# Kernel tuning notes

Hardware: AMD Instinct MI355X
Metric: run time of the kernel (lower is better)

Reference implementation:

```python
import jax, jax.numpy as jnp
import numpy as np

B, HH, WW, C, HEADS = 8, 56, 56, 384, 6
DIM_OUT = 384


def _upsample2x_bilinear(x):
    # x: [..., m, n] -> [..., 2m, 2n]; matches torch F.interpolate bilinear align_corners=False
    m, n = x.shape[-2], x.shape[-1]
    def coords(inn):
        c = (jnp.arange(2 * inn) + 0.5) / 2.0 - 0.5
        c = jnp.clip(c, 0.0, inn - 1)
        i0 = jnp.floor(c).astype(jnp.int32)
        i1 = jnp.minimum(i0 + 1, inn - 1)
        return i0, i1, (c - i0).astype(x.dtype)
    i0, i1, wy = coords(m)
    j0, j1, wx = coords(n)
    rows = x[..., i0, :] * (1 - wy)[:, None] + x[..., i1, :] * wy[:, None]
    return rows[..., :, j0] * (1 - wx) + rows[..., :, j1] * wx


def setup_inputs() -> dict:
    key = jax.random.key(0)
    ks = jax.random.split(key, 12)
    inp = {
        'x': jax.random.normal(ks[0], (B, HH * WW, C), jnp.float32),
        'res_attn': jax.random.normal(ks[1], (B, HEADS, (HH // 4) * (WW // 4), (HH // 2) * (WW // 2)), jnp.float32),
        'conv_q_w': jax.random.normal(ks[2], (C, 1, 3, 3), jnp.float32) * 0.05,
        'ln_g': jnp.ones((C,), jnp.float32),
        'ln_b': jnp.zeros((C,), jnp.float32),
        'wq': jax.random.normal(ks[3], (DIM_OUT, C), jnp.float32) * 0.02,
        'wk': jax.random.normal(ks[4], (DIM_OUT, C), jnp.float32) * 0.02,
        'wv': jax.random.normal(ks[5], (DIM_OUT, C), jnp.float32) * 0.02,
        'w_proj': jax.random.normal(ks[6], (DIM_OUT, DIM_OUT), jnp.float32) * 0.02,
        'b_proj': jnp.zeros((DIM_OUT,), jnp.float32),
        'w_fuse': jax.random.normal(ks[7], (HEADS, 2 * HEADS, 1, 1), jnp.float32) * 0.1,
        'b_fuse': jnp.zeros((HEADS,), jnp.float32),
        'h': HH,
        'w': WW,
    }
    return inp


def reference(x, res_attn, conv_q_w, ln_g, ln_b, wq, wk, wv, w_proj, b_proj, w_fuse, b_fuse, h, w):
    Bz, _, Cc = x.shape
    heads = w_fuse.shape[0]
    xi = x.transpose(0, 2, 1).reshape(Bz, Cc, h, w)  # b c h w
    # conv_proj_q: depthwise conv k3 s2 p1 (no bias), then LayerNorm
    q = jax.lax.conv_general_dilated(
        xi, conv_q_w, (2, 2), ((1, 1), (1, 1)),
        dimension_numbers=('NCHW', 'OIHW', 'NCHW'), feature_group_count=Cc)
    hq, wq2 = q.shape[2], q.shape[3]
    q = q.reshape(Bz, Cc, hq * wq2).transpose(0, 2, 1)  # b t c
    mu = q.mean(-1, keepdims=True)
    var = ((q - mu) ** 2).mean(-1, keepdims=True)
    q = (q - mu) / jnp.sqrt(var + 1e-5) * ln_g + ln_b
    # conv_proj_k/v: avg pool k2 s2 p0
    kv = xi.reshape(Bz, Cc, h // 2, 2, w // 2, 2).mean(axis=(3, 5))
    kv = kv.reshape(Bz, Cc, (h // 2) * (w // 2)).transpose(0, 2, 1)  # b t c
    dim_out = wq.shape[0]
    dh = dim_out // heads
    def split(t):
        return t.reshape(Bz, t.shape[1], heads, dh).transpose(0, 2, 1, 3)
    qh = split(q @ wq.T)
    kh = split(kv @ wk.T)
    vh = split(kv @ wv.T)
    scale = dim_out ** -0.5
    attn_score = jnp.einsum('bhlk,bhtk->bhlt', qh, kh) * scale  # [B,H,L,T]
    sh, sw = h // 4, w // 4
    a = res_attn.shape[-1]
    rx = res_attn[:, :, :sh * sw, :]
    rx = rx.reshape(Bz * heads, sh * sw, a).transpose(0, 2, 1).reshape(Bz * heads, a, sh, sw)
    rx = _upsample2x_bilinear(rx)  # (b h) a 2sh 2sw
    rx = rx.reshape(Bz, heads, a, 4 * sh * sw).transpose(0, 1, 3, 2)  # b h L a
    cat = jnp.concatenate([attn_score, rx], axis=1)  # [B, 2H, L, T]
    attn_score = jnp.einsum('bclt,oc->bolt', cat, w_fuse[:, :, 0, 0]) + b_fuse[None, :, None, None]
    attn = jax.nn.softmax(attn_score, axis=-1)
    out = jnp.einsum('bhlt,bhtv->bhlv', attn, vh)
    out = out.transpose(0, 2, 1, 3).reshape(Bz, -1, dim_out)
    return out @ w_proj.T + b_proj
```

## Files before the change

kernel.cpp:

```cpp
#include <hip/hip_runtime.h>

typedef unsigned int uint;
typedef unsigned short ushort_t;
typedef short bf16x8 __attribute__((ext_vector_type(8)));
typedef float f32x4 __attribute__((ext_vector_type(4)));

__device__ __forceinline__ ushort_t f2bf(float f) {
  uint u = __builtin_bit_cast(uint, f);
  u += 0x7fffu + ((u >> 16) & 1u);
  return (ushort_t)(u >> 16);
}
__device__ __forceinline__ float bf2f(ushort_t s) {
  return __builtin_bit_cast(float, (uint)s << 16);
}
__device__ __forceinline__ bf16x8 ld_frag(const ushort_t* p) {
  return __builtin_bit_cast(bf16x8, *(const uint4*)p);
}

__global__ __launch_bounds__(384) void k_convln(
    const float* __restrict__ x, const float* __restrict__ wc,
    const float* __restrict__ g, const float* __restrict__ bb,
    ushort_t* __restrict__ qout)
{
  const int b  = blockIdx.x / 784;
  const int t  = blockIdx.x % 784;
  const int oy = t / 28, ox = t % 28;
  const int c  = threadIdx.x;
  const float* xb = x + (size_t)b * 3136 * 384 + c;
  float acc = 0.f;
  #pragma unroll
  for (int ky = 0; ky < 3; ky++) {
    const int iy = 2 * oy - 1 + ky;
    if (iy < 0 || iy >= 56) continue;
    #pragma unroll
    for (int kx = 0; kx < 3; kx++) {
      const int ix = 2 * ox - 1 + kx;
      if (ix < 0 || ix >= 56) continue;
      acc += wc[c * 9 + ky * 3 + kx] * xb[(size_t)(iy * 56 + ix) * 384];
    }
  }
  float s = acc, s2 = acc * acc;
  #pragma unroll
  for (int off = 32; off >= 1; off >>= 1) {
    s  += __shfl_xor(s,  off);
    s2 += __shfl_xor(s2, off);
  }
  __shared__ float ps[6], ps2[6];
  if ((c & 63) == 0) { ps[c >> 6] = s; ps2[c >> 6] = s2; }
  __syncthreads();
  float S = 0.f, S2 = 0.f;
  #pragma unroll
  for (int i = 0; i < 6; i++) { S += ps[i]; S2 += ps2[i]; }
  const float mu  = S * (1.f / 384.f);
  const float var = S2 * (1.f / 384.f) - mu * mu;
  const float inv = rsqrtf(var + 1e-5f);
  qout[((size_t)b * 784 + t) * 384 + c] = f2bf((acc - mu) * inv * g[c] + bb[c]);
}

__global__ __launch_bounds__(256) void k_pool(
    const float* __restrict__ x, ushort_t* __restrict__ kvout)
{
  const int idx = blockIdx.x * 256 + threadIdx.x;
  const int c = idx % 384;
  const int t = (idx / 384) % 784;
  const int b = idx / (384 * 784);
  const int ty = t / 28, tx = t % 28;
  const float* xb = x + (size_t)b * 3136 * 384 + c;
  const int r0 = (2 * ty) * 56 + 2 * tx;
  const float v = xb[(size_t)r0 * 384] + xb[(size_t)(r0 + 1) * 384]
                + xb[(size_t)(r0 + 56) * 384] + xb[(size_t)(r0 + 57) * 384];
  kvout[idx] = f2bf(v * 0.25f);
}

__global__ __launch_bounds__(256) void k_wcvt(
    const float* __restrict__ a, const float* __restrict__ b,
    const float* __restrict__ c, const float* __restrict__ d,
    ushort_t* __restrict__ oa, ushort_t* __restrict__ ob,
    ushort_t* __restrict__ oc, ushort_t* __restrict__ od)
{
  const int i = blockIdx.x * 256 + threadIdx.x;
  if (i < 147456) {
    oa[i] = f2bf(a[i]); ob[i] = f2bf(b[i]);
    oc[i] = f2bf(c[i]); od[i] = f2bf(d[i]);
  }
}

template<int MODE>
__global__ __launch_bounds__(256) void k_gemm(
    const ushort_t* __restrict__ X, const ushort_t* __restrict__ W,
    const float* __restrict__ bias, void* __restrict__ Y)
{
  __shared__ ushort_t As[128][40];
  __shared__ ushort_t Bs[128][40];
  const int tid = threadIdx.x, w = tid >> 6, lane = tid & 63;
  const int quad = lane >> 4, r = lane & 15;
  const int m0 = blockIdx.y * 128, n0 = blockIdx.x * 128;
  const int wm = w >> 1, wn = w & 1;
  const int lr = tid >> 2, lc = (tid & 3) << 3;
  const ushort_t* xp = X + (size_t)(m0 + lr) * 384 + lc;
  const ushort_t* wp = W + (size_t)(n0 + lr) * 384 + lc;
  f32x4 acc[4][4] = {};
  for (int k0 = 0; k0 < 384; k0 += 32) {
    __syncthreads();
    *(uint4*)&As[lr][lc]      = *(const uint4*)(xp + k0);
    *(uint4*)&As[lr + 64][lc] = *(const uint4*)(xp + (size_t)64 * 384 + k0);
    *(uint4*)&Bs[lr][lc]      = *(const uint4*)(wp + k0);
    *(uint4*)&Bs[lr + 64][lc] = *(const uint4*)(wp + (size_t)64 * 384 + k0);
    __syncthreads();
    bf16x8 af[4], bf_[4];
    #pragma unroll
    for (int mt = 0; mt < 4; mt++) af[mt]  = *(const bf16x8*)&As[wm * 64 + mt * 16 + r][quad * 8];
    #pragma unroll
    for (int nt = 0; nt < 4; nt++) bf_[nt] = *(const bf16x8*)&Bs[wn * 64 + nt * 16 + r][quad * 8];
    #pragma unroll
    for (int mt = 0; mt < 4; mt++)
      #pragma unroll
      for (int nt = 0; nt < 4; nt++)
        acc[mt][nt] = __builtin_amdgcn_mfma_f32_16x16x32_bf16(af[mt], bf_[nt], acc[mt][nt], 0, 0, 0);
  }
  #pragma unroll
  for (int mt = 0; mt < 4; mt++) {
    #pragma unroll
    for (int nt = 0; nt < 4; nt++) {
      #pragma unroll
      for (int i = 0; i < 4; i++) {
        const int row = m0 + wm * 64 + mt * 16 + quad * 4 + i;
        const int col = n0 + wn * 64 + nt * 16 + r;
        const float v = acc[mt][nt][i];
        if constexpr (MODE == 2) {
          ((float*)Y)[(size_t)row * 384 + col] = v + bias[col];
        } else if constexpr (MODE == 0) {
          ((ushort_t*)Y)[(size_t)row * 384 + col] = f2bf(v);
        } else {
          const int bb = row / 784, tt = row % 784;
          ((ushort_t*)Y)[((size_t)bb * 384 + col) * 784 + tt] = f2bf(v);
        }
      }
    }
  }
}

__global__ __launch_bounds__(256) void k_qk(
    const ushort_t* __restrict__ Qb, const ushort_t* __restrict__ Kb,
    ushort_t* __restrict__ S)
{
  const int tid = threadIdx.x, w = tid >> 6, lane = tid & 63;
  const int quad = lane >> 4, r = lane & 15;
  const int bh = blockIdx.z, b = bh / 6, h = bh % 6;
  const int m0 = blockIdx.y * 64 + w * 16;
  const int t0 = blockIdx.x * 112;
  const int lq = min(m0 + r, 783);
  const ushort_t* qp = Qb + (size_t)(b * 784 + lq) * 384 + h * 64 + quad * 8;
  const bf16x8 a0 = ld_frag(qp), a1 = ld_frag(qp + 32);
  f32x4 acc[7] = {};
  #pragma unroll
  for (int j = 0; j < 7; j++) {
    const int t = t0 + j * 16 + r;
    const ushort_t* kp = Kb + (size_t)(b * 784 + t) * 384 + h * 64 + quad * 8;
    acc[j] = __builtin_amdgcn_mfma_f32_16x16x32_bf16(a0, ld_frag(kp),      acc[j], 0, 0, 0);
    acc[j] = __builtin_amdgcn_mfma_f32_16x16x32_bf16(a1, ld_frag(kp + 32), acc[j], 0, 0, 0);
  }
  const float scale = 0.05103103630798288f;
  #pragma unroll
  for (int j = 0; j < 7; j++) {
    #pragma unroll
    for (int i = 0; i < 4; i++) {
      const int lo = m0 + quad * 4 + i;
      if (lo < 784)
        S[((size_t)(b * 784 + lo) * 6 + h) * 784 + t0 + j * 16 + r] = f2bf(acc[j][i] * scale);
    }
  }
}

__global__ __launch_bounds__(256) void k_fuse(
    ushort_t* __restrict__ S, const float* __restrict__ ra,
    const float* __restrict__ w_fuse, const float* __restrict__ b_fuse)
{
  const int tid = threadIdx.x;
  const int bl = blockIdx.x, b = bl / 784, l = bl % 784;
  __shared__ float wf[72], bfu[6];
  __shared__ float redm[4][6], reds[4][6];
  if (tid < 72) wf[tid] = w_fuse[tid];
  if (tid < 6)  bfu[tid] = b_fuse[tid];
  __syncthreads();

  const int Y = l / 28, X = l % 28;
  const float cy = fminf(fmaxf((float)Y * 0.5f - 0.25f, 0.f), 13.f);
  const float cx = fminf(fmaxf((float)X * 0.5f - 0.25f, 0.f), 13.f);
  const int y0 = (int)cy, y1 = min(y0 + 1, 13);
  const int x0 = (int)cx, x1 = min(x0 + 1, 13);
  const float fy = cy - (float)y0, fx = cx - (float)x0;
  const float w00 = (1.f - fy) * (1.f - fx), w01 = (1.f - fy) * fx;
  const float w10 = fy * (1.f - fx),         w11 = fy * fx;
  const int p00 = (y0 * 14 + x0) * 784, p01 = (y0 * 14 + x1) * 784;
  const int p10 = (y1 * 14 + x0) * 784, p11 = (y1 * 14 + x1) * 784;

  ushort_t* Srow = S + (size_t)bl * 6 * 784;
  const float* rab = ra + (size_t)b * 6 * 196 * 784;

  float F[4][6];
  #pragma unroll
  for (int j = 0; j < 4; j++) {
    const int t = tid + j * 256;
    if (t < 784) {
      float a[6];
      #pragma unroll
      for (int o = 0; o < 6; o++) a[o] = bfu[o];
      #pragma unroll
      for (int c = 0; c < 6; c++) {
        const float* rc = rab + (size_t)c * (196 * 784);
        const float rx = w00 * rc[p00 + t] + w01 * rc[p01 + t]
                       + w10 * rc[p10 + t] + w11 * rc[p11 + t];
        const float sv = bf2f(Srow[c * 784 + t]);
        #pragma unroll
        for (int o = 0; o < 6; o++) a[o] += wf[o * 12 + c] * sv + wf[o * 12 + 6 + c] * rx;
      }
      #pragma unroll
      for (int o = 0; o < 6; o++) F[j][o] = a[o];
    } else {
      #pragma unroll
      for (int o = 0; o < 6; o++) F[j][o] = -1e30f;
    }
  }
  float mx[6];
  #pragma unroll
  for (int o = 0; o < 6; o++) {
    mx[o] = fmaxf(fmaxf(F[0][o], F[1][o]), fmaxf(F[2][o], F[3][o]));
    #pragma unroll
    for (int off = 32; off >= 1; off >>= 1) mx[o] = fmaxf(mx[o], __shfl_xor(mx[o], off));
  }
  if ((tid & 63) == 0) {
    #pragma unroll
    for (int o = 0; o < 6; o++) redm[tid >> 6][o] = mx[o];
  }
  __syncthreads();
  float M[6];
  #pragma unroll
  for (int o = 0; o < 6; o++)
    M[o] = fmaxf(fmaxf(redm[0][o], redm[1][o]), fmaxf(redm[2][o], redm[3][o]));
  float sm[6] = {};
  #pragma unroll
  for (int j = 0; j < 4; j++)
    #pragma unroll
    for (int o = 0; o < 6; o++) {
      const float p = __expf(F[j][o] - M[o]);
      F[j][o] = p; sm[o] += p;
    }
  #pragma unroll
  for (int o = 0; o < 6; o++) {
    #pragma unroll
    for (int off = 32; off >= 1; off >>= 1) sm[o] += __shfl_xor(sm[o], off);
  }
  if ((tid & 63) == 0) {
    #pragma unroll
    for (int o = 0; o < 6; o++) reds[tid >> 6][o] = sm[o];
  }
  __syncthreads();
  float inv[6];
  #pragma unroll
  for (int o = 0; o < 6; o++)
    inv[o] = 1.f / (reds[0][o] + reds[1][o] + reds[2][o] + reds[3][o]);
  #pragma unroll
  for (int j = 0; j < 4; j++) {
    const int t = tid + j * 256;
    if (t < 784) {
      #pragma unroll
      for (int o = 0; o < 6; o++) Srow[o * 784 + t] = f2bf(F[j][o] * inv[o]);
    }
  }
}

__global__ __launch_bounds__(256) void k_pv(
    const ushort_t* __restrict__ P, const ushort_t* __restrict__ Vt,
    ushort_t* __restrict__ O)
{
  const int tid = threadIdx.x, w = tid >> 6, lane = tid & 63;
  const int quad = lane >> 4, r = lane & 15;
  const int bo = blockIdx.y, b = bo / 6, o = bo % 6;
  const int m0 = blockIdx.x * 64 + w * 16;
  const int lq = min(m0 + r, 783);
  const ushort_t* ap = P + ((size_t)(b * 784 + lq) * 6 + o) * 784 + quad * 8;
  const ushort_t* bp = Vt + ((size_t)b * 384 + o * 64 + r) * 784 + quad * 8;
  f32x4 acc[4] = {};
  for (int kk = 0; kk < 25; kk++) {
    const int k0 = kk * 32;
    const bool full = (kk < 24) | (quad < 2);
    bf16x8 af = {}, bf_[4] = {};
    if (full) {
      af = ld_frag(ap + k0);
      #pragma unroll
      for (int nt = 0; nt < 4; nt++) bf_[nt] = ld_frag(bp + (size_t)nt * 16 * 784 + k0);
    }
    #pragma unroll
    for (int nt = 0; nt < 4; nt++)
      acc[nt] = __builtin_amdgcn_mfma_f32_16x16x32_bf16(af, bf_[nt], acc[nt], 0, 0, 0);
  }
  #pragma unroll
  for (int nt = 0; nt < 4; nt++) {
    #pragma unroll
    for (int i = 0; i < 4; i++) {
      const int lo = m0 + quad * 4 + i;
      if (lo < 784)
        O[(size_t)(b * 784 + lo) * 384 + o * 64 + nt * 16 + r] = f2bf(acc[nt][i]);
    }
  }
}

extern "C" void kernel_launch(void* const* d_in, const int* in_sizes, int n_in,
                              void* d_out, int out_size, void* d_ws, size_t ws_size,
                              hipStream_t stream)
{
  const float* x        = (const float*)d_in[0];
  const float* res_attn = (const float*)d_in[1];
  const float* conv_w   = (const float*)d_in[2];
  const float* ln_g     = (const float*)d_in[3];
  const float* ln_b     = (const float*)d_in[4];
  const float* wq       = (const float*)d_in[5];
  const float* wk       = (const float*)d_in[6];
  const float* wv       = (const float*)d_in[7];
  const float* w_proj   = (const float*)d_in[8];
  const float* b_proj   = (const float*)d_in[9];
  const float* w_fuse   = (const float*)d_in[10];
  const float* b_fuse   = (const float*)d_in[11];
  float* out = (float*)d_out;

  const size_t NE = (size_t)8 * 784 * 384;
  const size_t NW = 147456;
  ushort_t* q_ln_b = (ushort_t*)d_ws;
  ushort_t* kv_b   = q_ln_b + NE;
  ushort_t* Qb     = kv_b + NE;
  ushort_t* Kb     = Qb + NE;
  ushort_t* Vt     = Kb + NE;
  ushort_t* Opre   = Vt + NE;
  ushort_t* wqb    = Opre + NE;
  ushort_t* wkb    = wqb + NW;
  ushort_t* wvb    = wkb + NW;
  ushort_t* wpb    = wvb + NW;
  ushort_t* S      = wpb + NW;

  k_convln<<<dim3(8 * 784), dim3(384), 0, stream>>>(x, conv_w, ln_g, ln_b, q_ln_b);
  k_pool  <<<dim3(9408),    dim3(256), 0, stream>>>(x, kv_b);
  k_wcvt  <<<dim3(576),     dim3(256), 0, stream>>>(wq, wk, wv, w_proj, wqb, wkb, wvb, wpb);

  k_gemm<0><<<dim3(3, 49), dim3(256), 0, stream>>>(q_ln_b, wqb, nullptr, Qb);
  k_gemm<0><<<dim3(3, 49), dim3(256), 0, stream>>>(kv_b,   wkb, nullptr, Kb);
  k_gemm<1><<<dim3(3, 49), dim3(256), 0, stream>>>(kv_b,   wvb, nullptr, Vt);

  k_qk  <<<dim3(7, 13, 48), dim3(256), 0, stream>>>(Qb, Kb, S);
  k_fuse<<<dim3(8 * 784),   dim3(256), 0, stream>>>(S, res_attn, w_fuse, b_fuse);
  k_pv  <<<dim3(13, 48),    dim3(256), 0, stream>>>(S, Vt, Opre);

  k_gemm<2><<<dim3(3, 49), dim3(256), 0, stream>>>(Opre, wpb, b_proj, out);
}
```

Before: 328.7 us.

## Fuse QK, head-mixing softmax and PV into one flash-style kernel

Replaces the three attention kernels (QK scores, fuse+softmax, PV) with one kernel that keeps scores in registers. It runs an online softmax with a lazy rescale threshold and combines per-wave partial results through shared memory. A new pre-pass mixes res_attn across heads by w_fuse before upsampling, which is valid because the bilinear upsample is linear. The goal is to drop the large bf16 S round-trips through global memory. In exchange, the grid is only 392 blocks of 16 query rows, K and V are re-read for every row block, and a full-size fp32 Z buffer is written and then gathered with four taps per element.

```diff
diff --git a/kernel.cpp b/kernel.cpp
--- a/kernel.cpp
+++ b/kernel.cpp
@@ -15,6 +15,10 @@
 }
 __device__ __forceinline__ bf16x8 ld_frag(const ushort_t* p) {
   return __builtin_bit_cast(bf16x8, *(const uint4*)p);
+}
+__device__ __forceinline__ float uload(const float* p) {
+  return __builtin_bit_cast(float,
+      __builtin_amdgcn_readfirstlane(__builtin_bit_cast(int, *p)));
 }
 
 __global__ __launch_bounds__(384) void k_convln(
@@ -140,169 +144,209 @@
   }
 }
 
-__global__ __launch_bounds__(256) void k_qk(
+__global__ __launch_bounds__(256) void k_premix(
+    const float* __restrict__ ra, const float* __restrict__ w_fuse,
+    float* __restrict__ Z)
+{
+  const int NP = 196 * 784 / 4;
+  const int idx = blockIdx.x * 256 + threadIdx.x;
+  if (idx >= 8 * NP) return;
+  const int b = idx / NP, st = idx % NP;
+  const f32x4* rb = (const f32x4*)(ra + (size_t)b * 6 * 153664) + st;
+  f32x4 v[6];
+  #pragma unroll
+  for (int c = 0; c < 6; c++) v[c] = rb[(size_t)c * NP];
+  f32x4* zb = (f32x4*)(Z + (size_t)b * 6 * 153664) + st;
+  #pragma unroll
+  for (int o = 0; o < 6; o++) {
+    f32x4 acc = {};
+    #pragma unroll
+    for (int c = 0; c < 6; c++) acc += uload(w_fuse + o * 12 + 6 + c) * v[c];
+    zb[(size_t)o * NP] = acc;
+  }
+}
+
+__global__ __launch_bounds__(256, 2) void k_flash(
     const ushort_t* __restrict__ Qb, const ushort_t* __restrict__ Kb,
-    ushort_t* __restrict__ S)
+    const ushort_t* __restrict__ Vt, const float* __restrict__ Z,
+    const float* __restrict__ w_fuse, const float* __restrict__ b_fuse,
+    ushort_t* __restrict__ O)
 {
   const int tid = threadIdx.x, w = tid >> 6, lane = tid & 63;
   const int quad = lane >> 4, r = lane & 15;
-  const int bh = blockIdx.z, b = bh / 6, h = bh % 6;
-  const int m0 = blockIdx.y * 64 + w * 16;
-  const int t0 = blockIdx.x * 112;
-  const int lq = min(m0 + r, 783);
-  const ushort_t* qp = Qb + (size_t)(b * 784 + lq) * 384 + h * 64 + quad * 8;
-  const bf16x8 a0 = ld_frag(qp), a1 = ld_frag(qp + 32);
-  f32x4 acc[7] = {};
-  #pragma unroll
-  for (int j = 0; j < 7; j++) {
-    const int t = t0 + j * 16 + r;
-    const ushort_t* kp = Kb + (size_t)(b * 784 + t) * 384 + h * 64 + quad * 8;
-    acc[j] = __builtin_amdgcn_mfma_f32_16x16x32_bf16(a0, ld_frag(kp),      acc[j], 0, 0, 0);
-    acc[j] = __builtin_amdgcn_mfma_f32_16x16x32_bf16(a1, ld_frag(kp + 32), acc[j], 0, 0, 0);
-  }
-  const float scale = 0.05103103630798288f;
-  #pragma unroll
-  for (int j = 0; j < 7; j++) {
-    #pragma unroll
-    for (int i = 0; i < 4; i++) {
-      const int lo = m0 + quad * 4 + i;
-      if (lo < 784)
-        S[((size_t)(b * 784 + lo) * 6 + h) * 784 + t0 + j * 16 + r] = f2bf(acc[j][i] * scale);
-    }
-  }
-}
-
-__global__ __launch_bounds__(256) void k_fuse(
-    ushort_t* __restrict__ S, const float* __restrict__ ra,
-    const float* __restrict__ w_fuse, const float* __restrict__ b_fuse)
-{
-  const int tid = threadIdx.x;
-  const int bl = blockIdx.x, b = bl / 784, l = bl % 784;
-  __shared__ float wf[72], bfu[6];
-  __shared__ float redm[4][6], reds[4][6];
-  if (tid < 72) wf[tid] = w_fuse[tid];
-  if (tid < 6)  bfu[tid] = b_fuse[tid];
+  const int b  = blockIdx.y;
+  const int l0 = blockIdx.x * 16;
+
+  __shared__ ushort_t Qs[16][424];
+  __shared__ ushort_t Pl[4][16][40];
+  __shared__ float accbuf[4][16][64];
+  __shared__ float sbuf[4][16];
+  __shared__ float wmbuf[4][6];
+
+  #pragma unroll
+  for (int c = 0; c < 3; c++) {
+    const int idx = c * 256 + tid;
+    const int row = idx / 48, col8 = idx % 48;
+    *(uint4*)&Qs[row][col8 * 8] =
+        *(const uint4*)(Qb + ((size_t)(b * 784 + l0 + row)) * 384 + col8 * 8);
+  }
   __syncthreads();
 
-  const int Y = l / 28, X = l % 28;
-  const float cy = fminf(fmaxf((float)Y * 0.5f - 0.25f, 0.f), 13.f);
-  const float cx = fminf(fmaxf((float)X * 0.5f - 0.25f, 0.f), 13.f);
-  const int y0 = (int)cy, y1 = min(y0 + 1, 13);
-  const int x0 = (int)cx, x1 = min(x0 + 1, 13);
-  const float fy = cy - (float)y0, fx = cx - (float)x0;
-  const float w00 = (1.f - fy) * (1.f - fx), w01 = (1.f - fy) * fx;
-  const float w10 = fy * (1.f - fx),         w11 = fy * fx;
-  const int p00 = (y0 * 14 + x0) * 784, p01 = (y0 * 14 + x1) * 784;
-  const int p10 = (y1 * 14 + x0) * 784, p11 = (y1 * 14 + x1) * 784;
-
-  ushort_t* Srow = S + (size_t)bl * 6 * 784;
-  const float* rab = ra + (size_t)b * 6 * 196 * 784;
-
-  float F[4][6];
-  #pragma unroll
-  for (int j = 0; j < 4; j++) {
-    const int t = tid + j * 256;
-    if (t < 784) {
-      float a[6];
-      #pragma unroll
-      for (int o = 0; o < 6; o++) a[o] = bfu[o];
-      #pragma unroll
-      for (int c = 0; c < 6; c++) {
-        const float* rc = rab + (size_t)c * (196 * 784);
-        const float rx = w00 * rc[p00 + t] + w01 * rc[p01 + t]
-                       + w10 * rc[p10 + t] + w11 * rc[p11 + t];
-        const float sv = bf2f(Srow[c * 784 + t]);
+  float wfs[6][6], bfu[6];
+  #pragma unroll
+  for (int o = 0; o < 6; o++) {
+    bfu[o] = uload(b_fuse + o);
+    #pragma unroll
+    for (int h = 0; h < 6; h++)
+      wfs[o][h] = uload(w_fuse + o * 12 + h) * 0.05103103630798288f;
+  }
+
+  int p00a[4], p01a[4], p10a[4];
+  float fxa[4], fya[4];
+  #pragma unroll
+  for (int i = 0; i < 4; i++) {
+    const int l = l0 + quad * 4 + i;
+    const int Y = l / 28, X = l % 28;
+    const float cy = fminf(fmaxf((float)Y * 0.5f - 0.25f, 0.f), 13.f);
+    const float cx = fminf(fmaxf((float)X * 0.5f - 0.25f, 0.f), 13.f);
+    const int y0 = (int)cy, y1 = min(y0 + 1, 13);
+    const int x0 = (int)cx, x1 = min(x0 + 1, 13);
+    fya[i] = cy - (float)y0;
+    fxa[i] = cx - (float)x0;
+    p00a[i] = (y0 * 14 + x0) * 784;
+    p01a[i] = (y0 * 14 + x1) * 784;
+    p10a[i] = (y1 * 14 + x0) * 784;
+  }
+
+  f32x4 accp[6][4] = {};
+  float srow[6][4] = {};
+  float mo[6];
+  #pragma unroll
+  for (int o = 0; o < 6; o++) mo[o] = -1e30f;
+
+  for (int tt = w; tt < 25; tt += 4) {
+    const int t0 = tt * 32;
+    const int nj = (t0 + 32 <= 784) ? 2 : 1;
+
+    f32x4 accs[6][2] = {};
+    #pragma unroll
+    for (int j = 0; j < 2; j++) {
+      if (j < nj) {
+        const ushort_t* kp = Kb + ((size_t)(b * 784 + t0 + j * 16 + r)) * 384;
         #pragma unroll
-        for (int o = 0; o < 6; o++) a[o] += wf[o * 12 + c] * sv + wf[o * 12 + 6 + c] * rx;
-      }
-      #pragma unroll
-      for (int o = 0; o < 6; o++) F[j][o] = a[o];
-    } else {
-      #pragma unroll
-      for (int o = 0; o < 6; o++) F[j][o] = -1e30f;
-    }
-  }
-  float mx[6];
+        for (int h = 0; h < 6; h++) {
+          const bf16x8 a0 = *(const bf16x8*)&Qs[r][h * 64 + quad * 8];
+          const bf16x8 a1 = *(const bf16x8*)&Qs[r][h * 64 + 32 + quad * 8];
+          accs[h][j] = __builtin_amdgcn_mfma_f32_16x16x32_bf16(
+              a0, ld_frag(kp + h * 64 + quad * 8),      accs[h][j], 0, 0, 0);
+          accs[h][j] = __builtin_amdgcn_mfma_f32_16x16x32_bf16(
+              a1, ld_frag(kp + h * 64 + 32 + quad * 8), accs[h][j], 0, 0, 0);
+        }
+      }
+    }
+
+    #pragma unroll
+    for (int o = 0; o < 6; o++) {
+      const float* zo = Z + ((size_t)(b * 6 + o)) * 153664;
+      float f[2][4];
+      #pragma unroll
+      for (int j = 0; j < 2; j++) {
+        if (j < nj) {
+          const int t = t0 + j * 16 + r;
+          #pragma unroll
+          for (int i = 0; i < 4; i++) {
+            float v = bfu[o];
+            #pragma unroll
+            for (int h = 0; h < 6; h++) v += wfs[o][h] * accs[h][j][i];
+            const float z00 = zo[p00a[i] + t];
+            const float z01 = zo[p01a[i] + t];
+            const float z10 = zo[p10a[i] + t];
+            const float z11 = zo[p10a[i] + p01a[i] - p00a[i] + t];
+            const float r0 = z00 + fxa[i] * (z01 - z00);
+            const float r1 = z10 + fxa[i] * (z11 - z10);
+            f[j][i] = v + r0 + fya[i] * (r1 - r0);
+          }
+        } else {
+          #pragma unroll
+          for (int i = 0; i < 4; i++) f[j][i] = -1e30f;
+        }
+      }
+      float mx = fmaxf(fmaxf(fmaxf(f[0][0], f[0][1]), fmaxf(f[0][2], f[0][3])),
+                       fmaxf(fmaxf(f[1][0], f[1][1]), fmaxf(f[1][2], f[1][3])));
+      #pragma unroll
+      for (int off = 32; off >= 1; off >>= 1)
+        mx = fmaxf(mx, __shfl_xor(mx, off));
+      if (mx > mo[o] + 8.f) {
+        const float sc = __expf(mo[o] - mx);
+        mo[o] = mx;
+        #pragma unroll
+        for (int nt = 0; nt < 4; nt++) accp[o][nt] *= sc;
+        #pragma unroll
+        for (int i = 0; i < 4; i++) srow[o][i] *= sc;
+      }
+      #pragma unroll
+      for (int j = 0; j < 2; j++) {
+        #pragma unroll
+        for (int i = 0; i < 4; i++) {
+          const float p = __expf(f[j][i] - mo[o]);
+          srow[o][i] += p;
+          Pl[w][quad * 4 + i][j * 16 + r] = f2bf(p);
+        }
+      }
+      const bf16x8 pa = *(const bf16x8*)&Pl[w][r][quad * 8];
+      const int vt0 = min(t0 + quad * 8, 776);
+      const ushort_t* vp = Vt + ((size_t)(b * 384 + o * 64 + r)) * 784 + vt0;
+      #pragma unroll
+      for (int nt = 0; nt < 4; nt++)
+        accp[o][nt] = __builtin_amdgcn_mfma_f32_16x16x32_bf16(
+            pa, ld_frag(vp + (size_t)nt * 16 * 784), accp[o][nt], 0, 0, 0);
+    }
+  }
+
+  #pragma unroll
+  for (int o = 0; o < 6; o++)
+    #pragma unroll
+    for (int i = 0; i < 4; i++)
+      #pragma unroll
+      for (int m = 1; m <= 8; m <<= 1)
+        srow[o][i] += __shfl_xor(srow[o][i], m);
+
+  if (lane == 0) {
+    #pragma unroll
+    for (int o = 0; o < 6; o++) wmbuf[w][o] = mo[o];
+  }
+  __syncthreads();
+
+  const int orow = tid >> 4, ocol = (tid & 15) << 2;
   #pragma unroll
   for (int o = 0; o < 6; o++) {
-    mx[o] = fmaxf(fmaxf(F[0][o], F[1][o]), fmaxf(F[2][o], F[3][o]));
-    #pragma unroll
-    for (int off = 32; off >= 1; off >>= 1) mx[o] = fmaxf(mx[o], __shfl_xor(mx[o], off));
-  }
-  if ((tid & 63) == 0) {
-    #pragma unroll
-    for (int o = 0; o < 6; o++) redm[tid >> 6][o] = mx[o];
-  }
-  __syncthreads();
-  float M[6];
-  #pragma unroll
-  for (int o = 0; o < 6; o++)
-    M[o] = fmaxf(fmaxf(redm[0][o], redm[1][o]), fmaxf(redm[2][o], redm[3][o]));
-  float sm[6] = {};
-  #pragma unroll
-  for (int j = 0; j < 4; j++)
-    #pragma unroll
-    for (int o = 0; o < 6; o++) {
-      const float p = __expf(F[j][o] - M[o]);
-      F[j][o] = p; sm[o] += p;
-    }
-  #pragma unroll
-  for (int o = 0; o < 6; o++) {
-    #pragma unroll
-    for (int off = 32; off >= 1; off >>= 1) sm[o] += __shfl_xor(sm[o], off);
-  }
-  if ((tid & 63) == 0) {
-    #pragma unroll
-    for (int o = 0; o < 6; o++) reds[tid >> 6][o] = sm[o];
-  }
-  __syncthreads();
-  float inv[6];
-  #pragma unroll
-  for (int o = 0; o < 6; o++)
-    inv[o] = 1.f / (reds[0][o] + reds[1][o] + reds[2][o] + reds[3][o]);
-  #pragma unroll
-  for (int j = 0; j < 4; j++) {
-    const int t = tid + j * 256;
-    if (t < 784) {
-      #pragma unroll
-      for (int o = 0; o < 6; o++) Srow[o * 784 + t] = f2bf(F[j][o] * inv[o]);
-    }
-  }
-}
-
-__global__ __launch_bounds__(256) void k_pv(
-    const ushort_t* __restrict__ P, const ushort_t* __restrict__ Vt,
-    ushort_t* __restrict__ O)
-{
-  const int tid = threadIdx.x, w = tid >> 6, lane = tid & 63;
-  const int quad = lane >> 4, r = lane & 15;
-  const int bo = blockIdx.y, b = bo / 6, o = bo % 6;
-  const int m0 = blockIdx.x * 64 + w * 16;
-  const int lq = min(m0 + r, 783);
-  const ushort_t* ap = P + ((size_t)(b * 784 + lq) * 6 + o) * 784 + quad * 8;
-  const ushort_t* bp = Vt + ((size_t)b * 384 + o * 64 + r) * 784 + quad * 8;
-  f32x4 acc[4] = {};
-  for (int kk = 0; kk < 25; kk++) {
-    const int k0 = kk * 32;
-    const bool full = (kk < 24) | (quad < 2);
-    bf16x8 af = {}, bf_[4] = {};
-    if (full) {
-      af = ld_frag(ap + k0);
-      #pragma unroll
-      for (int nt = 0; nt < 4; nt++) bf_[nt] = ld_frag(bp + (size_t)nt * 16 * 784 + k0);
-    }
+    const float M = fmaxf(fmaxf(wmbuf[0][o], wmbuf[1][o]),
+                          fmaxf(wmbuf[2][o], wmbuf[3][o]));
+    const float ew = __expf(mo[o] - M);
     #pragma unroll
     for (int nt = 0; nt < 4; nt++)
-      acc[nt] = __builtin_amdgcn_mfma_f32_16x16x32_bf16(af, bf_[nt], acc[nt], 0, 0, 0);
-  }
-  #pragma unroll
-  for (int nt = 0; nt < 4; nt++) {
-    #pragma unroll
-    for (int i = 0; i < 4; i++) {
-      const int lo = m0 + quad * 4 + i;
-      if (lo < 784)
-        O[(size_t)(b * 784 + lo) * 384 + o * 64 + nt * 16 + r] = f2bf(acc[nt][i]);
-    }
+      #pragma unroll
+      for (int i = 0; i < 4; i++)
+        accbuf[w][quad * 4 + i][nt * 16 + r] = accp[o][nt][i] * ew;
+    if (r == 0) {
+      #pragma unroll
+      for (int i = 0; i < 4; i++) sbuf[w][quad * 4 + i] = srow[o][i] * ew;
+    }
+    __syncthreads();
+    const float st = sbuf[0][orow] + sbuf[1][orow] + sbuf[2][orow] + sbuf[3][orow];
+    const float inv = 1.f / st;
+    ushort_t pk[4];
+    #pragma unroll
+    for (int e = 0; e < 4; e++) {
+      const float v = (accbuf[0][orow][ocol + e] + accbuf[1][orow][ocol + e]
+                     + accbuf[2][orow][ocol + e] + accbuf[3][orow][ocol + e]) * inv;
+      pk[e] = f2bf(v);
+    }
+    uint2 w2;
+    w2.x = (uint)pk[0] | ((uint)pk[1] << 16);
+    w2.y = (uint)pk[2] | ((uint)pk[3] << 16);
+    *(uint2*)(O + ((size_t)(b * 784) + l0 + orow) * 384 + o * 64 + ocol) = w2;
+    __syncthreads();
   }
 }
 
@@ -336,8 +380,9 @@
   ushort_t* wkb    = wqb + NW;
   ushort_t* wvb    = wkb + NW;
   ushort_t* wpb    = wvb + NW;
-  ushort_t* S      = wpb + NW;
-
+  float*    Z      = (float*)(wpb + NW);
+
+  k_premix<<<dim3(1201),   dim3(256), 0, stream>>>(res_attn, w_fuse, Z);
   k_convln<<<dim3(8 * 784), dim3(384), 0, stream>>>(x, conv_w, ln_g, ln_b, q_ln_b);
   k_pool  <<<dim3(9408),    dim3(256), 0, stream>>>(x, kv_b);
   k_wcvt  <<<dim3(576),     dim3(256), 0, stream>>>(wq, wk, wv, w_proj, wqb, wkb, wvb, wpb);
@@ -346,9 +391,7 @@
   k_gemm<0><<<dim3(3, 49), dim3(256), 0, stream>>>(kv_b,   wkb, nullptr, Kb);
   k_gemm<1><<<dim3(3, 49), dim3(256), 0, stream>>>(kv_b,   wvb, nullptr, Vt);
 
-  k_qk  <<<dim3(7, 13, 48), dim3(256), 0, stream>>>(Qb, Kb, S);
-  k_fuse<<<dim3(8 * 784),   dim3(256), 0, stream>>>(S, res_attn, w_fuse, b_fuse);
-  k_pv  <<<dim3(13, 48),    dim3(256), 0, stream>>>(S, Vt, Opre);
+  k_flash<<<dim3(49, 8), dim3(256), 0, stream>>>(Qb, Kb, Vt, Z, w_fuse, b_fuse, Opre);
 
   k_gemm<2><<<dim3(3, 49), dim3(256), 0, stream>>>(Opre, wpb, b_proj, out);
 }
```

New measurement: 470.4 us. +43.1%, slower.

## Fold head-mixing into QK GEMM and fuse softmax into PV

Applied to the files above, without the earlier changes.

The 1x1 head fuse is linear, so the score half of the mix is moved into the QK GEMM by scaling Q per input head and contracting over all 384 channels for each output head. The residual-attention half is premixed once in a separate pass and then bilinearly sampled in the score epilogue. Softmax normalization moves into the PV kernel, which exponentiates scores without subtracting a max (clamped at 60) and divides by the row sum afterwards. The batch runs in two halves so the score buffer fits the workspace. This removes the separate fuse/softmax pass over S but does 6x more QK MFMA work, adds a full fp32 Z round-trip, and risks precision loss from the missing max subtraction.

```diff
diff --git a/kernel.cpp b/kernel.cpp
--- a/kernel.cpp
+++ b/kernel.cpp
@@ -15,6 +15,10 @@
 }
 __device__ __forceinline__ bf16x8 ld_frag(const ushort_t* p) {
   return __builtin_bit_cast(bf16x8, *(const uint4*)p);
+}
+__device__ __forceinline__ float uload(const float* p) {
+  return __builtin_bit_cast(float,
+      __builtin_amdgcn_readfirstlane(__builtin_bit_cast(int, *p)));
 }
 
 __global__ __launch_bounds__(384) void k_convln(
@@ -140,168 +144,169 @@
   }
 }
 
-__global__ __launch_bounds__(256) void k_qk(
+__global__ __launch_bounds__(256) void k_premix(
+    const float* __restrict__ ra, const float* __restrict__ w_fuse,
+    float* __restrict__ Z)
+{
+  const int NP = 196 * 784 / 4;
+  const int idx = blockIdx.x * 256 + threadIdx.x;
+  if (idx >= 8 * NP) return;
+  const int b = idx / NP, st = idx % NP;
+  const f32x4* rb = (const f32x4*)(ra + (size_t)b * 6 * 153664) + st;
+  f32x4 v[6];
+  #pragma unroll
+  for (int c = 0; c < 6; c++) v[c] = rb[(size_t)c * NP];
+  f32x4* zb = (f32x4*)(Z + (size_t)b * 6 * 153664) + st;
+  #pragma unroll
+  for (int o = 0; o < 6; o++) {
+    f32x4 acc = {};
+    #pragma unroll
+    for (int c = 0; c < 6; c++) acc += uload(w_fuse + o * 12 + 6 + c) * v[c];
+    zb[(size_t)o * NP] = acc;
+  }
+}
+
+__global__ __launch_bounds__(256) void k_score(
     const ushort_t* __restrict__ Qb, const ushort_t* __restrict__ Kb,
-    ushort_t* __restrict__ S)
-{
+    const float* __restrict__ Z, const float* __restrict__ w_fuse,
+    const float* __restrict__ b_fuse, ushort_t* __restrict__ S, int b0)
+{
+  __shared__ ushort_t Bs[64][424];
   const int tid = threadIdx.x, w = tid >> 6, lane = tid & 63;
   const int quad = lane >> 4, r = lane & 15;
-  const int bh = blockIdx.z, b = bh / 6, h = bh % 6;
+  const int bo = blockIdx.z, o = bo % 6, b = b0 + bo / 6;
   const int m0 = blockIdx.y * 64 + w * 16;
-  const int t0 = blockIdx.x * 112;
+  const int t0 = blockIdx.x * 64;
+
+  #pragma unroll
+  for (int cc = 0; cc < 12; cc++) {
+    const int idx = cc * 256 + tid;
+    const int row = idx / 48, col8 = idx % 48;
+    const int tr = min(t0 + row, 783);
+    *(uint4*)&Bs[row][col8 * 8] =
+        *(const uint4*)(Kb + ((size_t)(b * 784 + tr)) * 384 + col8 * 8);
+  }
+
   const int lq = min(m0 + r, 783);
-  const ushort_t* qp = Qb + (size_t)(b * 784 + lq) * 384 + h * 64 + quad * 8;
-  const bf16x8 a0 = ld_frag(qp), a1 = ld_frag(qp + 32);
-  f32x4 acc[7] = {};
-  #pragma unroll
-  for (int j = 0; j < 7; j++) {
+  const ushort_t* qp = Qb + ((size_t)(b * 784 + lq)) * 384 + quad * 8;
+  float wfs[6];
+  #pragma unroll
+  for (int c = 0; c < 6; c++)
+    wfs[c] = uload(w_fuse + o * 12 + c) * 0.05103103630798288f;
+  bf16x8 a[12];
+  #pragma unroll
+  for (int ks = 0; ks < 12; ks++) {
+    uint4 v = *(const uint4*)(qp + (size_t)ks * 32);
+    const ushort_t* sv = (const ushort_t*)&v;
+    ushort_t ov[8];
+    #pragma unroll
+    for (int e = 0; e < 8; e++) ov[e] = f2bf(bf2f(sv[e]) * wfs[ks >> 1]);
+    a[ks] = __builtin_bit_cast(bf16x8, *(uint4*)ov);
+  }
+  __syncthreads();
+
+  f32x4 acc[4] = {};
+  #pragma unroll
+  for (int j = 0; j < 4; j++)
+    #pragma unroll
+    for (int ks = 0; ks < 12; ks++)
+      acc[j] = __builtin_amdgcn_mfma_f32_16x16x32_bf16(
+          a[ks], *(const bf16x8*)&Bs[j * 16 + r][ks * 32 + quad * 8],
+          acc[j], 0, 0, 0);
+
+  const float bfu = uload(b_fuse + o);
+  const float* zo = Z + ((size_t)(b * 6 + o)) * 153664;
+  int p00a[4], p01a[4], p10a[4];
+  float fxa[4], fya[4];
+  #pragma unroll
+  for (int i = 0; i < 4; i++) {
+    const int l = m0 + quad * 4 + i;
+    const int Y = l / 28, X = l % 28;
+    const float cy = fminf(fmaxf((float)Y * 0.5f - 0.25f, 0.f), 13.f);
+    const float cx = fminf(fmaxf((float)X * 0.5f - 0.25f, 0.f), 13.f);
+    const int y0 = (int)cy, y1 = min(y0 + 1, 13);
+    const int x0 = (int)cx, x1 = min(x0 + 1, 13);
+    fya[i] = cy - (float)y0;
+    fxa[i] = cx - (float)x0;
+    p00a[i] = (y0 * 14 + x0) * 784;
+    p01a[i] = (y0 * 14 + x1) * 784;
+    p10a[i] = (y1 * 14 + x0) * 784;
+  }
+  #pragma unroll
+  for (int j = 0; j < 4; j++) {
     const int t = t0 + j * 16 + r;
-    const ushort_t* kp = Kb + (size_t)(b * 784 + t) * 384 + h * 64 + quad * 8;
-    acc[j] = __builtin_amdgcn_mfma_f32_16x16x32_bf16(a0, ld_frag(kp),      acc[j], 0, 0, 0);
-    acc[j] = __builtin_amdgcn_mfma_f32_16x16x32_bf16(a1, ld_frag(kp + 32), acc[j], 0, 0, 0);
-  }
-  const float scale = 0.05103103630798288f;
-  #pragma unroll
-  for (int j = 0; j < 7; j++) {
+    if (t < 784) {
+      #pragma unroll
+      for (int i = 0; i < 4; i++) {
+        const int lo = m0 + quad * 4 + i;
+        if (lo < 784) {
+          const float z00 = zo[p00a[i] + t];
+          const float z01 = zo[p01a[i] + t];
+          const float z10 = zo[p10a[i] + t];
+          const float z11 = zo[p10a[i] + p01a[i] - p00a[i] + t];
+          const float r0 = z00 + fxa[i] * (z01 - z00);
+          const float r1 = z10 + fxa[i] * (z11 - z10);
+          S[((size_t)bo * 784 + lo) * 784 + t] =
+              f2bf(acc[j][i] + bfu + r0 + fya[i] * (r1 - r0));
+        }
+      }
+    }
+  }
+}
+
+__global__ __launch_bounds__(64) void k_pvs(
+    const ushort_t* __restrict__ S, const ushort_t* __restrict__ Vt,
+    ushort_t* __restrict__ O, int b0)
+{
+  const int lane = threadIdx.x;
+  const int quad = lane >> 4, r = lane & 15;
+  const int bo = blockIdx.y, o = bo % 6, b = b0 + bo / 6;
+  const int m0 = blockIdx.x * 16;
+  const int lq = min(m0 + r, 783);
+  const ushort_t* ap = S + ((size_t)bo * 784 + lq) * 784 + quad * 8;
+  const ushort_t* bp = Vt + ((size_t)(b * 384 + o * 64 + r)) * 784 + quad * 8;
+  f32x4 acc[4] = {};
+  float psv[8] = {};
+  for (int kk = 0; kk < 25; kk++) {
+    const int k0 = kk * 32;
+    const bool full = (kk < 24) | (quad < 2);
+    bf16x8 pa = {};
+    bf16x8 bfr[4] = {};
+    if (full) {
+      uint4 sv4 = *(const uint4*)(ap + k0);
+      const ushort_t* sv = (const ushort_t*)&sv4;
+      ushort_t pv[8];
+      #pragma unroll
+      for (int e = 0; e < 8; e++) {
+        const float p = __expf(fminf(bf2f(sv[e]), 60.f));
+        psv[e] += p;
+        pv[e] = f2bf(p);
+      }
+      pa = __builtin_bit_cast(bf16x8, *(uint4*)pv);
+      #pragma unroll
+      for (int nt = 0; nt < 4; nt++)
+        bfr[nt] = ld_frag(bp + (size_t)nt * 16 * 784 + k0);
+    }
+    #pragma unroll
+    for (int nt = 0; nt < 4; nt++)
+      acc[nt] = __builtin_amdgcn_mfma_f32_16x16x32_bf16(pa, bfr[nt], acc[nt], 0, 0, 0);
+  }
+  float psum = 0.f;
+  #pragma unroll
+  for (int e = 0; e < 8; e++) psum += psv[e];
+  psum += __shfl_xor(psum, 16);
+  psum += __shfl_xor(psum, 32);
+  float inv[4];
+  #pragma unroll
+  for (int i = 0; i < 4; i++) inv[i] = 1.f / __shfl(psum, quad * 4 + i);
+  #pragma unroll
+  for (int nt = 0; nt < 4; nt++) {
     #pragma unroll
     for (int i = 0; i < 4; i++) {
       const int lo = m0 + quad * 4 + i;
       if (lo < 784)
-        S[((size_t)(b * 784 + lo) * 6 + h) * 784 + t0 + j * 16 + r] = f2bf(acc[j][i] * scale);
-    }
-  }
-}
-
-__global__ __launch_bounds__(256) void k_fuse(
-    ushort_t* __restrict__ S, const float* __restrict__ ra,
-    const float* __restrict__ w_fuse, const float* __restrict__ b_fuse)
-{
-  const int tid = threadIdx.x;
-  const int bl = blockIdx.x, b = bl / 784, l = bl % 784;
-  __shared__ float wf[72], bfu[6];
-  __shared__ float redm[4][6], reds[4][6];
-  if (tid < 72) wf[tid] = w_fuse[tid];
-  if (tid < 6)  bfu[tid] = b_fuse[tid];
-  __syncthreads();
-
-  const int Y = l / 28, X = l % 28;
-  const float cy = fminf(fmaxf((float)Y * 0.5f - 0.25f, 0.f), 13.f);
-  const float cx = fminf(fmaxf((float)X * 0.5f - 0.25f, 0.f), 13.f);
-  const int y0 = (int)cy, y1 = min(y0 + 1, 13);
-  const int x0 = (int)cx, x1 = min(x0 + 1, 13);
-  const float fy = cy - (float)y0, fx = cx - (float)x0;
-  const float w00 = (1.f - fy) * (1.f - fx), w01 = (1.f - fy) * fx;
-  const float w10 = fy * (1.f - fx),         w11 = fy * fx;
-  const int p00 = (y0 * 14 + x0) * 784, p01 = (y0 * 14 + x1) * 784;
-  const int p10 = (y1 * 14 + x0) * 784, p11 = (y1 * 14 + x1) * 784;
-
-  ushort_t* Srow = S + (size_t)bl * 6 * 784;
-  const float* rab = ra + (size_t)b * 6 * 196 * 784;
-
-  float F[4][6];
-  #pragma unroll
-  for (int j = 0; j < 4; j++) {
-    const int t = tid + j * 256;
-    if (t < 784) {
-      float a[6];
-      #pragma unroll
-      for (int o = 0; o < 6; o++) a[o] = bfu[o];
-      #pragma unroll
-      for (int c = 0; c < 6; c++) {
-        const float* rc = rab + (size_t)c * (196 * 784);
-        const float rx = w00 * rc[p00 + t] + w01 * rc[p01 + t]
-                       + w10 * rc[p10 + t] + w11 * rc[p11 + t];
-        const float sv = bf2f(Srow[c * 784 + t]);
-        #pragma unroll
-        for (int o = 0; o < 6; o++) a[o] += wf[o * 12 + c] * sv + wf[o * 12 + 6 + c] * rx;
-      }
-      #pragma unroll
-      for (int o = 0; o < 6; o++) F[j][o] = a[o];
-    } else {
-      #pragma unroll
-      for (int o = 0; o < 6; o++) F[j][o] = -1e30f;
-    }
-  }
-  float mx[6];
-  #pragma unroll
-  for (int o = 0; o < 6; o++) {
-    mx[o] = fmaxf(fmaxf(F[0][o], F[1][o]), fmaxf(F[2][o], F[3][o]));
-    #pragma unroll
-    for (int off = 32; off >= 1; off >>= 1) mx[o] = fmaxf(mx[o], __shfl_xor(mx[o], off));
-  }
-  if ((tid & 63) == 0) {
-    #pragma unroll
-    for (int o = 0; o < 6; o++) redm[tid >> 6][o] = mx[o];
-  }
-  __syncthreads();
-  float M[6];
-  #pragma unroll
-  for (int o = 0; o < 6; o++)
-    M[o] = fmaxf(fmaxf(redm[0][o], redm[1][o]), fmaxf(redm[2][o], redm[3][o]));
-  float sm[6] = {};
-  #pragma unroll
-  for (int j = 0; j < 4; j++)
-    #pragma unroll
-    for (int o = 0; o < 6; o++) {
-      const float p = __expf(F[j][o] - M[o]);
-      F[j][o] = p; sm[o] += p;
-    }
-  #pragma unroll
-  for (int o = 0; o < 6; o++) {
-    #pragma unroll
-    for (int off = 32; off >= 1; off >>= 1) sm[o] += __shfl_xor(sm[o], off);
-  }
-  if ((tid & 63) == 0) {
-    #pragma unroll
-    for (int o = 0; o < 6; o++) reds[tid >> 6][o] = sm[o];
-  }
-  __syncthreads();
-  float inv[6];
-  #pragma unroll
-  for (int o = 0; o < 6; o++)
-    inv[o] = 1.f / (reds[0][o] + reds[1][o] + reds[2][o] + reds[3][o]);
-  #pragma unroll
-  for (int j = 0; j < 4; j++) {
-    const int t = tid + j * 256;
-    if (t < 784) {
-      #pragma unroll
-      for (int o = 0; o < 6; o++) Srow[o * 784 + t] = f2bf(F[j][o] * inv[o]);
-    }
-  }
-}
-
-__global__ __launch_bounds__(256) void k_pv(
-    const ushort_t* __restrict__ P, const ushort_t* __restrict__ Vt,
-    ushort_t* __restrict__ O)
-{
-  const int tid = threadIdx.x, w = tid >> 6, lane = tid & 63;
-  const int quad = lane >> 4, r = lane & 15;
-  const int bo = blockIdx.y, b = bo / 6, o = bo % 6;
-  const int m0 = blockIdx.x * 64 + w * 16;
-  const int lq = min(m0 + r, 783);
-  const ushort_t* ap = P + ((size_t)(b * 784 + lq) * 6 + o) * 784 + quad * 8;
-  const ushort_t* bp = Vt + ((size_t)b * 384 + o * 64 + r) * 784 + quad * 8;
-  f32x4 acc[4] = {};
-  for (int kk = 0; kk < 25; kk++) {
-    const int k0 = kk * 32;
-    const bool full = (kk < 24) | (quad < 2);
-    bf16x8 af = {}, bf_[4] = {};
-    if (full) {
-      af = ld_frag(ap + k0);
-      #pragma unroll
-      for (int nt = 0; nt < 4; nt++) bf_[nt] = ld_frag(bp + (size_t)nt * 16 * 784 + k0);
-    }
-    #pragma unroll
-    for (int nt = 0; nt < 4; nt++)
-      acc[nt] = __builtin_amdgcn_mfma_f32_16x16x32_bf16(af, bf_[nt], acc[nt], 0, 0, 0);
-  }
-  #pragma unroll
-  for (int nt = 0; nt < 4; nt++) {
-    #pragma unroll
-    for (int i = 0; i < 4; i++) {
-      const int lo = m0 + quad * 4 + i;
-      if (lo < 784)
-        O[(size_t)(b * 784 + lo) * 384 + o * 64 + nt * 16 + r] = f2bf(acc[nt][i]);
+        O[((size_t)(b * 784 + lo)) * 384 + o * 64 + nt * 16 + r] =
+            f2bf(acc[nt][i] * inv[i]);
     }
   }
 }
@@ -326,18 +331,21 @@
 
   const size_t NE = (size_t)8 * 784 * 384;
   const size_t NW = 147456;
-  ushort_t* q_ln_b = (ushort_t*)d_ws;
-  ushort_t* kv_b   = q_ln_b + NE;
-  ushort_t* Qb     = kv_b + NE;
-  ushort_t* Kb     = Qb + NE;
-  ushort_t* Vt     = Kb + NE;
-  ushort_t* Opre   = Vt + NE;
-  ushort_t* wqb    = Opre + NE;
-  ushort_t* wkb    = wqb + NW;
-  ushort_t* wvb    = wkb + NW;
-  ushort_t* wpb    = wvb + NW;
-  ushort_t* S      = wpb + NW;
-
+  const size_t NS = (size_t)4 * 6 * 784 * 784;
+  ushort_t* Qb   = (ushort_t*)d_ws;
+  ushort_t* Kb   = Qb + NE;
+  ushort_t* Vt   = Kb + NE;
+  ushort_t* Opre = Vt + NE;
+  ushort_t* wqb  = Opre + NE;
+  ushort_t* wkb  = wqb + NW;
+  ushort_t* wvb  = wkb + NW;
+  ushort_t* wpb  = wvb + NW;
+  float*    Z    = (float*)(wpb + NW);
+  ushort_t* S_f  = (ushort_t*)(Z + (size_t)8 * 6 * 153664);
+  ushort_t* q_ln_b = S_f;
+  ushort_t* kv_b   = S_f + NE;
+
+  k_premix<<<dim3(1201),    dim3(256), 0, stream>>>(res_attn, w_fuse, Z);
   k_convln<<<dim3(8 * 784), dim3(384), 0, stream>>>(x, conv_w, ln_g, ln_b, q_ln_b);
   k_pool  <<<dim3(9408),    dim3(256), 0, stream>>>(x, kv_b);
   k_wcvt  <<<dim3(576),     dim3(256), 0, stream>>>(wq, wk, wv, w_proj, wqb, wkb, wvb, wpb);
@@ -346,9 +354,11 @@
   k_gemm<0><<<dim3(3, 49), dim3(256), 0, stream>>>(kv_b,   wkb, nullptr, Kb);
   k_gemm<1><<<dim3(3, 49), dim3(256), 0, stream>>>(kv_b,   wvb, nullptr, Vt);
 
-  k_qk  <<<dim3(7, 13, 48), dim3(256), 0, stream>>>(Qb, Kb, S);
-  k_fuse<<<dim3(8 * 784),   dim3(256), 0, stream>>>(S, res_attn, w_fuse, b_fuse);
-  k_pv  <<<dim3(13, 48),    dim3(256), 0, stream>>>(S, Vt, Opre);
+  for (int h = 0; h < 2; h++) {
+    k_score<<<dim3(13, 13, 24), dim3(256), 0, stream>>>(
+        Qb, Kb, Z, w_fuse, b_fuse, S_f, h * 4);
+    k_pvs<<<dim3(49, 24), dim3(64), 0, stream>>>(S_f, Vt, Opre, h * 4);
+  }
 
   k_gemm<2><<<dim3(3, 49), dim3(256), 0, stream>>>(Opre, wpb, b_proj, out);
 }
```

After: 397.6 us. 21.0% more time.
